# Kernel tuning notes

Hardware: AMD Instinct MI355X
Metric: run time of the kernel (lower is better)

## Reference

```python
import jax, jax.numpy as jnp
import numpy as np

B, S, D, H = 2, 2048, 1024, 16
HD = D // H  # head_dim = 64


def setup_inputs() -> dict:
    key = jax.random.key(0)
    ks = jax.random.split(key, 9)
    scale = 0.02
    x = jax.random.normal(ks[0], (B, S, D), dtype=jnp.float32)
    wq = jax.random.normal(ks[1], (D, D), dtype=jnp.float32) * scale
    bq = jnp.zeros((D,), dtype=jnp.float32)
    wk = jax.random.normal(ks[2], (D, D), dtype=jnp.float32) * scale
    bk = jnp.zeros((D,), dtype=jnp.float32)
    wv = jax.random.normal(ks[3], (D, D), dtype=jnp.float32) * scale
    bv = jnp.zeros((D,), dtype=jnp.float32)
    wo = jax.random.normal(ks[4], (D, D), dtype=jnp.float32) * scale
    bo = jnp.zeros((D,), dtype=jnp.float32)
    # causal mask: 1.0 where key position is in the future of query position
    mask = jnp.triu(jnp.ones((S, S), dtype=jnp.float32), k=1)[None, None]  # [1,1,S,S]
    return {"x": x, "wq": wq, "bq": bq, "wk": wk, "bk": bk,
            "wv": wv, "bv": bv, "wo": wo, "bo": bo, "mask": mask}


def reference(x, wq, bq, wk, bk, wv, bv, wo, bo, mask):
    b, s, d = x.shape
    q = (x @ wq + bq).reshape(b, s, H, HD).transpose(0, 2, 1, 3)  # [b,h,s,hd]
    k = (x @ wk + bk).reshape(b, s, H, HD).transpose(0, 2, 1, 3)
    v = (x @ wv + bv).reshape(b, s, H, HD).transpose(0, 2, 1, 3)
    scores = jnp.einsum('bhqd,bhkd->bhqk', q, k) / jnp.sqrt(jnp.float32(HD))
    scores = scores + mask * (-1e9)
    probs = jax.nn.softmax(scores, axis=-1)
    out = jnp.einsum('bhqk,bhkd->bhqd', probs, v)
    out = out.transpose(0, 2, 1, 3).reshape(b, s, d)
    return out @ wo + bo
```

## Files before the change

### kernel.cpp

```cpp
#include <hip/hip_runtime.h>
#include <hip/hip_bf16.h>
#include <cstdint>

#define DEV static __device__ __forceinline__

typedef unsigned short u16t;
typedef __attribute__((ext_vector_type(4))) float f32x4;
typedef __attribute__((ext_vector_type(4))) unsigned short u16x4;
typedef __attribute__((ext_vector_type(8))) unsigned short u16x8;
typedef __attribute__((ext_vector_type(8))) __bf16 bf16x8;

DEV u16t f2bf(float f) {
  unsigned u = __builtin_bit_cast(unsigned, f);
  u += 0x7fffu + ((u >> 16) & 1u);
  return (u16t)(u >> 16);
}
DEV float bf2f(u16t h) {
  unsigned u = ((unsigned)h) << 16;
  return __builtin_bit_cast(float, u);
}

DEV void gload_lds16(const void* g, void* l) {
  __builtin_amdgcn_global_load_lds(
      (const __attribute__((address_space(1))) void*)g,
      (__attribute__((address_space(3))) void*)l, 16, 0, 0);
}

DEV bf16x8 ldsfrag(const u16t* p) {
  return __builtin_bit_cast(bf16x8, *(const u16x8*)p);
}

__global__ __launch_bounds__(256) void k_convert_x(const float* __restrict__ x,
                                                   u16t* __restrict__ xb) {
  int i = (blockIdx.x * 256 + threadIdx.x) * 4;
  f32x4 v = *(const f32x4*)&x[i];
  u16x4 o;
#pragma unroll
  for (int j = 0; j < 4; ++j) o[j] = f2bf(v[j]);
  *(u16x4*)&xb[i] = o;
}

__global__ __launch_bounds__(256) void k_transw(const float* __restrict__ w0,
                                                const float* __restrict__ w1,
                                                const float* __restrict__ w2,
                                                const float* __restrict__ w3,
                                                u16t* __restrict__ qkvT,
                                                u16t* __restrict__ oT) {
  __shared__ float lds[64][68];
  int z = blockIdx.z;
  const float* W = (z == 0) ? w0 : (z == 1) ? w1 : (z == 2) ? w2 : w3;
  u16t* OUT = (z < 3) ? (qkvT + (size_t)z * 1024 * 1024) : oT;
  int k0 = blockIdx.x * 64, n0 = blockIdx.y * 64;
  int t = threadIdx.x;
  int kl = t >> 4, n4 = (t & 15) << 2;
#pragma unroll
  for (int p = 0; p < 4; ++p) {
    f32x4 v = *(const f32x4*)&W[(size_t)(k0 + kl + p * 16) * 1024 + n0 + n4];
    *(f32x4*)&lds[kl + p * 16][n4] = v;
  }
  __syncthreads();
  int nl = t >> 4, k4 = (t & 15) << 2;
#pragma unroll
  for (int p = 0; p < 4; ++p) {
    int n = nl + p * 16;
    u16x4 o;
#pragma unroll
    for (int i = 0; i < 4; ++i) o[i] = f2bf(lds[k4 + i][n]);
    *(u16x4*)&OUT[(size_t)(n0 + n) * 1024 + k0 + k4] = o;
  }
}

template <bool BF16_OUT>
__global__ __launch_bounds__(256) void k_gemm_bt(const u16t* __restrict__ A,
                                                 const u16t* __restrict__ BT,
                                                 void* __restrict__ Cout,
                                                 const float* __restrict__ b0,
                                                 const float* __restrict__ b1,
                                                 const float* __restrict__ b2,
                                                 int M, int N, int K) {
  __shared__ u16t Al[128 * 64];
  __shared__ u16t Bl[128 * 64];
  const int tid = threadIdx.x;
  const int l = tid & 63;
  const int w = tid >> 6;
  const int m0 = blockIdx.x * 128, n0 = blockIdx.y * 128;
  const int wm = (w >> 1) * 64, wn = (w & 1) * 64;
  const int lm = l & 15, lh = l >> 4;
  f32x4 acc[4][4] = {};

  const int nt = K >> 6;
  for (int t = 0; t < nt; ++t) {
    const int k0 = t << 6;
#pragma unroll
    for (int s = 0; s < 4; ++s) {
      int c = s * 256 + tid;
      int row = c >> 3, slot = c & 7;
      int ks = k0 + (((slot ^ (row & 7)) & 7) << 3);
      gload_lds16(A + (size_t)(m0 + row) * K + ks, &Al[c * 8]);
    }
#pragma unroll
    for (int s = 0; s < 4; ++s) {
      int c = s * 256 + tid;
      int row = c >> 3, slot = c & 7;
      int ks = k0 + (((slot ^ (row & 7)) & 7) << 3);
      gload_lds16(BT + (size_t)(n0 + row) * K + ks, &Bl[c * 8]);
    }
    asm volatile("s_waitcnt vmcnt(0)" ::: "memory");
    __syncthreads();

#pragma unroll
    for (int kk = 0; kk < 2; ++kk) {
      bf16x8 af[4], bfr[4];
#pragma unroll
      for (int i = 0; i < 4; ++i) {
        int ra = wm + i * 16 + lm;
        int sa = (kk * 4 + lh) ^ (ra & 7);
        af[i] = ldsfrag(&Al[ra * 64 + sa * 8]);
        int rb = wn + i * 16 + lm;
        int sb = (kk * 4 + lh) ^ (rb & 7);
        bfr[i] = ldsfrag(&Bl[rb * 64 + sb * 8]);
      }
#pragma unroll
      for (int i = 0; i < 4; ++i)
#pragma unroll
        for (int j = 0; j < 4; ++j)
          acc[i][j] = __builtin_amdgcn_mfma_f32_16x16x32_bf16(af[i], bfr[j],
                                                              acc[i][j], 0, 0, 0);
    }
    __syncthreads();
  }

#pragma unroll
  for (int i = 0; i < 4; ++i) {
    int row = m0 + wm + i * 16 + (lh << 2);
#pragma unroll
    for (int j = 0; j < 4; ++j) {
      int col = n0 + wn + j * 16 + lm;
      const float* bp = (col < 1024) ? b0 : ((col < 2048) ? b1 : b2);
      float bias = bp[col & 1023];
#pragma unroll
      for (int r = 0; r < 4; ++r) {
        float v = acc[i][j][r] + bias;
        if (BF16_OUT)
          ((u16t*)Cout)[(size_t)(row + r) * N + col] = f2bf(v);
        else
          ((float*)Cout)[(size_t)(row + r) * N + col] = v;
      }
    }
  }
}

__global__ __launch_bounds__(256) void k_transv(const u16t* __restrict__ qkv,
                                                u16t* __restrict__ vt) {
  __shared__ u16t lds[64][80];
  int bh = blockIdx.y, b = bh >> 4, h = bh & 15;
  int s0 = blockIdx.x * 64;
  int t = threadIdx.x;
  int sl = t >> 2, d16 = (t & 3) << 4;
  const u16t* src = qkv + (size_t)(b * 2048 + s0 + sl) * 3072 + 2048 + h * 64 + d16;
  *(u16x8*)&lds[sl][d16] = *(const u16x8*)src;
  *(u16x8*)&lds[sl][d16 + 8] = *(const u16x8*)(src + 8);
  __syncthreads();
  int dl = t >> 2, s16 = (t & 3) << 4;
  u16x8 o0, o1;
#pragma unroll
  for (int i = 0; i < 8; ++i) o0[i] = lds[s16 + i][dl];
#pragma unroll
  for (int i = 0; i < 8; ++i) o1[i] = lds[s16 + 8 + i][dl];
  u16t* dst = vt + ((size_t)bh * 64 + dl) * 2048 + s0 + s16;
  *(u16x8*)&dst[0] = o0;
  *(u16x8*)&dst[8] = o1;
}

__global__ __launch_bounds__(256, 4) void k_attn(const u16t* __restrict__ qkv,
                                                 const u16t* __restrict__ vt,
                                                 u16t* __restrict__ outp) {
  __shared__ u16t Kl[2][4096];
  __shared__ u16t Vl[2][4096];
  __shared__ u16t Pl[4][1024];
  const int tid = threadIdx.x, l = tid & 63, w = tid >> 6;
  const int lm = l & 15, lh = l >> 4;
  const int bh = blockIdx.x, b = bh >> 4, h = bh & 15;
  const int y = blockIdx.y;
  const int kg = y >> 3, jj = y & 7;
  const int qt = kg * 8 + ((kg & 1) ? (7 - jj) : jj);
  const int q0 = qt * 64;
  const int nt = qt + 1;

  bf16x8 aq[2];
  const int qrow = q0 + w * 16 + lm;
#pragma unroll
  for (int kk = 0; kk < 2; ++kk) {
    const u16t* src = qkv + (size_t)(b * 2048 + qrow) * 3072 + h * 64 + kk * 32 + lh * 8;
    u16x8 v = *(const u16x8*)src;
    u16x8 o;
#pragma unroll
    for (int e = 0; e < 8; ++e) o[e] = f2bf(bf2f(v[e]) * 0.125f);
    aq[kk] = __builtin_bit_cast(bf16x8, o);
  }

  float mrun = -1e30f;
  float lsum = 0.f;
  f32x4 aco[4] = {};

  const u16t* Kg = qkv + (size_t)b * 2048 * 3072 + 1024 + h * 64;
  const u16t* Vg = vt + (size_t)bh * 64 * 2048;
  u16t* Pw = &Pl[w][0];

  auto stage = [&](int buf, int t) {
#pragma unroll
    for (int s = 0; s < 2; ++s) {
      int c = s * 256 + tid;
      int row = c >> 3, col = ((c & 7) ^ (row & 7)) << 3;
      gload_lds16(Kg + (size_t)(t * 64 + row) * 3072 + col, &Kl[buf][c * 8]);
    }
#pragma unroll
    for (int s = 0; s < 2; ++s) {
      int c = s * 256 + tid;
      int row = c >> 3, col = ((c & 7) ^ (row & 7)) << 3;
      gload_lds16(Vg + (size_t)row * 2048 + t * 64 + col, &Vl[buf][c * 8]);
    }
  };

  stage(0, 0);
  asm volatile("s_waitcnt vmcnt(0)" ::: "memory");
  __syncthreads();

  int buf = 0;
  for (int t = 0; t < nt; ++t) {
    if (t + 1 < nt) stage(buf ^ 1, t + 1);

    f32x4 accs[4] = {};
#pragma unroll
    for (int kk = 0; kk < 2; ++kk) {
      bf16x8 ak[4];
#pragma unroll
      for (int nk = 0; nk < 4; ++nk) {
        int rk = nk * 16 + lm;
        int s16 = (kk * 4 + lh) ^ (rk & 7);
        ak[nk] = ldsfrag(&Kl[buf][rk * 64 + s16 * 8]);
      }
      __builtin_amdgcn_s_setprio(1);
#pragma unroll
      for (int nk = 0; nk < 4; ++nk)
        accs[nk] = __builtin_amdgcn_mfma_f32_16x16x32_bf16(ak[nk], aq[kk],
                                                           accs[nk], 0, 0, 0);
      __builtin_amdgcn_s_setprio(0);
    }

    float vmax = -1e30f;
#pragma unroll
    for (int nk = 0; nk < 4; ++nk)
#pragma unroll
      for (int r = 0; r < 4; ++r) {
        int kvpos = t * 64 + nk * 16 + lh * 4 + r;
        float v = accs[nk][r];
        v = (kvpos > qrow) ? -1e30f : v;
        accs[nk][r] = v;
        vmax = fmaxf(vmax, v);
      }

    if (!__all(vmax <= mrun + 8.f)) {
      float rm = fmaxf(vmax, __shfl_xor(vmax, 16));
      rm = fmaxf(rm, __shfl_xor(rm, 32));
      float mnew = fmaxf(mrun, rm);
      float alpha = __expf(mrun - mnew);
      mrun = mnew;
      lsum *= alpha;
#pragma unroll
      for (int r = 0; r < 4; ++r) {
        float ar = __shfl(alpha, lh * 4 + r);
#pragma unroll
        for (int nd = 0; nd < 4; ++nd) aco[nd][r] *= ar;
      }
    }

#pragma unroll
    for (int nk = 0; nk < 4; ++nk) {
      u16x4 pb;
#pragma unroll
      for (int r = 0; r < 4; ++r) {
        float p = __expf(accs[nk][r] - mrun);
        lsum += p;
        pb[r] = f2bf(p);
      }
      int s16 = (nk * 2 + (lh >> 1)) ^ (lm & 7);
      *(u16x4*)&Pw[lm * 64 + s16 * 8 + (lh & 1) * 4] = pb;
    }

#pragma unroll
    for (int kk = 0; kk < 2; ++kk) {
      int s16p = (kk * 4 + lh) ^ (lm & 7);
      bf16x8 ap = ldsfrag(&Pw[lm * 64 + s16p * 8]);
      __builtin_amdgcn_s_setprio(1);
#pragma unroll
      for (int nd = 0; nd < 4; ++nd) {
        int rv = nd * 16 + lm;
        int s16v = (kk * 4 + lh) ^ (rv & 7);
        bf16x8 bv = ldsfrag(&Vl[buf][rv * 64 + s16v * 8]);
        aco[nd] = __builtin_amdgcn_mfma_f32_16x16x32_bf16(ap, bv, aco[nd], 0, 0, 0);
      }
      __builtin_amdgcn_s_setprio(0);
    }

    asm volatile("s_waitcnt vmcnt(0)" ::: "memory");
    __syncthreads();
    buf ^= 1;
  }

  lsum += __shfl_xor(lsum, 16);
  lsum += __shfl_xor(lsum, 32);
  float inv = 1.0f / lsum;
#pragma unroll
  for (int r = 0; r < 4; ++r) {
    float ir = __shfl(inv, lh * 4 + r);
    int row = q0 + w * 16 + lh * 4 + r;
#pragma unroll
    for (int nd = 0; nd < 4; ++nd) {
      int col = h * 64 + nd * 16 + lm;
      outp[(size_t)(b * 2048 + row) * 1024 + col] = f2bf(aco[nd][r] * ir);
    }
  }
}

extern "C" void kernel_launch(void* const* d_in, const int* in_sizes, int n_in,
                              void* d_out, int out_size, void* d_ws, size_t ws_size,
                              hipStream_t stream) {
  const float* x = (const float*)d_in[0];
  const float* wq = (const float*)d_in[1];
  const float* bq = (const float*)d_in[2];
  const float* wk = (const float*)d_in[3];
  const float* bk = (const float*)d_in[4];
  const float* wv = (const float*)d_in[5];
  const float* bv = (const float*)d_in[6];
  const float* wo = (const float*)d_in[7];
  const float* bo = (const float*)d_in[8];

  char* ws = (char*)d_ws;
  u16t* xb = (u16t*)ws;
  u16t* wqkvT = (u16t*)(ws + (8u << 20));
  u16t* woT = (u16t*)(ws + (14u << 20));
  u16t* qkv = (u16t*)(ws + (16u << 20));
  u16t* vt = (u16t*)(ws + (40u << 20));
  u16t* attn_out = xb;

  k_convert_x<<<4096, 256, 0, stream>>>(x, xb);
  k_transw<<<dim3(16, 16, 4), 256, 0, stream>>>(wq, wk, wv, wo, wqkvT, woT);
  k_gemm_bt<true><<<dim3(32, 24), 256, 0, stream>>>(xb, wqkvT, qkv, bq, bk, bv,
                                                    4096, 3072, 1024);
  k_transv<<<dim3(32, 32), 256, 0, stream>>>(qkv, vt);
  k_attn<<<dim3(32, 32), 256, 0, stream>>>(qkv, vt, attn_out);
  k_gemm_bt<false><<<dim3(32, 8), 256, 0, stream>>>(attn_out, woT, d_out, bo, bo,
                                                    bo, 4096, 1024, 1024);
}
```

Before: 130.1 us.

## Fuse V transpose into QKV GEMM epilogue and restructure attention blocks

The QKV GEMM epilogue now writes the V columns straight into the transposed [b,h,d,s] layout, which removes the separate transpose kernel and its extra pass over memory. The attention kernel drops to 128 threads, and each wave now handles 32 query rows with two MFMA streams that share every K/V fragment load. Each block processes a pair of causal query tiles (jp and 31-jp) to balance work, and the causal mask is applied only on the diagonal tile. P is packed with v_cvt_pk_bf16_f32. In exchange there are fewer blocks and more registers per wave, and the V epilogue stores are strided 8-byte writes.

```diff
diff --git a/kernel.cpp b/kernel.cpp
--- a/kernel.cpp
+++ b/kernel.cpp
@@ -70,13 +70,14 @@
   }
 }
 
-template <bool BF16_OUT>
+template <bool BF16_OUT, bool VSPLIT>
 __global__ __launch_bounds__(256) void k_gemm_bt(const u16t* __restrict__ A,
                                                  const u16t* __restrict__ BT,
                                                  void* __restrict__ Cout,
                                                  const float* __restrict__ b0,
                                                  const float* __restrict__ b1,
                                                  const float* __restrict__ b2,
+                                                 u16t* __restrict__ vt,
                                                  int M, int N, int K) {
   __shared__ u16t Al[128 * 64];
   __shared__ u16t Bl[128 * 64];
@@ -130,195 +131,231 @@
     __syncthreads();
   }
 
-#pragma unroll
-  for (int i = 0; i < 4; ++i) {
-    int row = m0 + wm + i * 16 + (lh << 2);
+  if (!VSPLIT || (n0 + wn) < 2048) {
+#pragma unroll
+    for (int i = 0; i < 4; ++i) {
+      int row = m0 + wm + i * 16 + (lh << 2);
+#pragma unroll
+      for (int j = 0; j < 4; ++j) {
+        int col = n0 + wn + j * 16 + lm;
+        const float* bp = (col < 1024) ? b0 : ((col < 2048) ? b1 : b2);
+        float bias = bp[col & 1023];
+#pragma unroll
+        for (int r = 0; r < 4; ++r) {
+          float v = acc[i][j][r] + bias;
+          if (BF16_OUT)
+            ((u16t*)Cout)[(size_t)(row + r) * N + col] = f2bf(v);
+          else
+            ((float*)Cout)[(size_t)(row + r) * N + col] = v;
+        }
+      }
+    }
+  } else {
+#pragma unroll
+    for (int i = 0; i < 4; ++i) {
+      int row = m0 + wm + i * 16 + (lh << 2);
+      int bidx = row >> 11, s0 = row & 2047;
 #pragma unroll
     for (int j = 0; j < 4; ++j) {
-      int col = n0 + wn + j * 16 + lm;
-      const float* bp = (col < 1024) ? b0 : ((col < 2048) ? b1 : b2);
-      float bias = bp[col & 1023];
-#pragma unroll
-      for (int r = 0; r < 4; ++r) {
-        float v = acc[i][j][r] + bias;
-        if (BF16_OUT)
-          ((u16t*)Cout)[(size_t)(row + r) * N + col] = f2bf(v);
-        else
-          ((float*)Cout)[(size_t)(row + r) * N + col] = v;
-      }
-    }
-  }
-}
-
-__global__ __launch_bounds__(256) void k_transv(const u16t* __restrict__ qkv,
-                                                u16t* __restrict__ vt) {
-  __shared__ u16t lds[64][80];
-  int bh = blockIdx.y, b = bh >> 4, h = bh & 15;
-  int s0 = blockIdx.x * 64;
-  int t = threadIdx.x;
-  int sl = t >> 2, d16 = (t & 3) << 4;
-  const u16t* src = qkv + (size_t)(b * 2048 + s0 + sl) * 3072 + 2048 + h * 64 + d16;
-  *(u16x8*)&lds[sl][d16] = *(const u16x8*)src;
-  *(u16x8*)&lds[sl][d16 + 8] = *(const u16x8*)(src + 8);
-  __syncthreads();
-  int dl = t >> 2, s16 = (t & 3) << 4;
-  u16x8 o0, o1;
-#pragma unroll
-  for (int i = 0; i < 8; ++i) o0[i] = lds[s16 + i][dl];
-#pragma unroll
-  for (int i = 0; i < 8; ++i) o1[i] = lds[s16 + 8 + i][dl];
-  u16t* dst = vt + ((size_t)bh * 64 + dl) * 2048 + s0 + s16;
-  *(u16x8*)&dst[0] = o0;
-  *(u16x8*)&dst[8] = o1;
-}
-
-__global__ __launch_bounds__(256, 4) void k_attn(const u16t* __restrict__ qkv,
-                                                 const u16t* __restrict__ vt,
-                                                 u16t* __restrict__ outp) {
+        int col = n0 + wn + j * 16 + lm;
+        int d = col - 2048;
+        int hh = d >> 6, dd = d & 63;
+        float bias = b2[d];
+        u16x4 o;
+#pragma unroll
+        for (int r = 0; r < 4; ++r) o[r] = f2bf(acc[i][j][r] + bias);
+        *(u16x4*)&vt[((size_t)((bidx * 16 + hh) * 64 + dd)) * 2048 + s0] = o;
+      }
+    }
+  }
+}
+
+__global__ __launch_bounds__(128) void k_attn(const u16t* __restrict__ qkv,
+                                              const u16t* __restrict__ vt,
+                                              u16t* __restrict__ outp) {
   __shared__ u16t Kl[2][4096];
   __shared__ u16t Vl[2][4096];
-  __shared__ u16t Pl[4][1024];
+  __shared__ u16t Pl[2][2][1024];
   const int tid = threadIdx.x, l = tid & 63, w = tid >> 6;
   const int lm = l & 15, lh = l >> 4;
   const int bh = blockIdx.x, b = bh >> 4, h = bh & 15;
-  const int y = blockIdx.y;
-  const int kg = y >> 3, jj = y & 7;
-  const int qt = kg * 8 + ((kg & 1) ? (7 - jj) : jj);
-  const int q0 = qt * 64;
-  const int nt = qt + 1;
-
-  bf16x8 aq[2];
-  const int qrow = q0 + w * 16 + lm;
-#pragma unroll
-  for (int kk = 0; kk < 2; ++kk) {
-    const u16t* src = qkv + (size_t)(b * 2048 + qrow) * 3072 + h * 64 + kk * 32 + lh * 8;
-    u16x8 v = *(const u16x8*)src;
-    u16x8 o;
-#pragma unroll
-    for (int e = 0; e < 8; ++e) o[e] = f2bf(bf2f(v[e]) * 0.125f);
-    aq[kk] = __builtin_bit_cast(bf16x8, o);
-  }
-
-  float mrun = -1e30f;
-  float lsum = 0.f;
-  f32x4 aco[4] = {};
+  const int jp = blockIdx.y;
 
   const u16t* Kg = qkv + (size_t)b * 2048 * 3072 + 1024 + h * 64;
   const u16t* Vg = vt + (size_t)bh * 64 * 2048;
-  u16t* Pw = &Pl[w][0];
-
-  auto stage = [&](int buf, int t) {
-#pragma unroll
-    for (int s = 0; s < 2; ++s) {
-      int c = s * 256 + tid;
-      int row = c >> 3, col = ((c & 7) ^ (row & 7)) << 3;
-      gload_lds16(Kg + (size_t)(t * 64 + row) * 3072 + col, &Kl[buf][c * 8]);
-    }
-#pragma unroll
-    for (int s = 0; s < 2; ++s) {
-      int c = s * 256 + tid;
-      int row = c >> 3, col = ((c & 7) ^ (row & 7)) << 3;
-      gload_lds16(Vg + (size_t)row * 2048 + t * 64 + col, &Vl[buf][c * 8]);
+
+  auto stage = [&](int bb, int t) {
+#pragma unroll
+    for (int s = 0; s < 4; ++s) {
+      int c = s * 128 + tid;
+      int row = c >> 3, slot = c & 7;
+      int col = ((slot ^ (row & 7)) & 7) << 3;
+      gload_lds16(Kg + (size_t)(t * 64 + row) * 3072 + col, &Kl[bb][c * 8]);
+    }
+#pragma unroll
+    for (int s = 0; s < 4; ++s) {
+      int c = s * 128 + tid;
+      int row = c >> 3, slot = c & 7;
+      int col = ((slot ^ (row & 7)) & 7) << 3;
+      gload_lds16(Vg + (size_t)row * 2048 + t * 64 + col, &Vl[bb][c * 8]);
     }
   };
 
-  stage(0, 0);
-  asm volatile("s_waitcnt vmcnt(0)" ::: "memory");
-  __syncthreads();
-
-  int buf = 0;
-  for (int t = 0; t < nt; ++t) {
-    if (t + 1 < nt) stage(buf ^ 1, t + 1);
-
-    f32x4 accs[4] = {};
-#pragma unroll
-    for (int kk = 0; kk < 2; ++kk) {
-      bf16x8 ak[4];
-#pragma unroll
-      for (int nk = 0; nk < 4; ++nk) {
-        int rk = nk * 16 + lm;
-        int s16 = (kk * 4 + lh) ^ (rk & 7);
-        ak[nk] = ldsfrag(&Kl[buf][rk * 64 + s16 * 8]);
-      }
-      __builtin_amdgcn_s_setprio(1);
-#pragma unroll
-      for (int nk = 0; nk < 4; ++nk)
-        accs[nk] = __builtin_amdgcn_mfma_f32_16x16x32_bf16(ak[nk], aq[kk],
-                                                           accs[nk], 0, 0, 0);
-      __builtin_amdgcn_s_setprio(0);
-    }
-
-    float vmax = -1e30f;
-#pragma unroll
-    for (int nk = 0; nk < 4; ++nk)
-#pragma unroll
-      for (int r = 0; r < 4; ++r) {
-        int kvpos = t * 64 + nk * 16 + lh * 4 + r;
-        float v = accs[nk][r];
-        v = (kvpos > qrow) ? -1e30f : v;
-        accs[nk][r] = v;
-        vmax = fmaxf(vmax, v);
-      }
-
-    if (!__all(vmax <= mrun + 8.f)) {
-      float rm = fmaxf(vmax, __shfl_xor(vmax, 16));
-      rm = fmaxf(rm, __shfl_xor(rm, 32));
-      float mnew = fmaxf(mrun, rm);
-      float alpha = __expf(mrun - mnew);
-      mrun = mnew;
-      lsum *= alpha;
-#pragma unroll
-      for (int r = 0; r < 4; ++r) {
-        float ar = __shfl(alpha, lh * 4 + r);
-#pragma unroll
-        for (int nd = 0; nd < 4; ++nd) aco[nd][r] *= ar;
-      }
-    }
-
-#pragma unroll
-    for (int nk = 0; nk < 4; ++nk) {
-      u16x4 pb;
-#pragma unroll
-      for (int r = 0; r < 4; ++r) {
-        float p = __expf(accs[nk][r] - mrun);
-        lsum += p;
-        pb[r] = f2bf(p);
-      }
-      int s16 = (nk * 2 + (lh >> 1)) ^ (lm & 7);
-      *(u16x4*)&Pw[lm * 64 + s16 * 8 + (lh & 1) * 4] = pb;
-    }
-
-#pragma unroll
-    for (int kk = 0; kk < 2; ++kk) {
-      int s16p = (kk * 4 + lh) ^ (lm & 7);
-      bf16x8 ap = ldsfrag(&Pw[lm * 64 + s16p * 8]);
-      __builtin_amdgcn_s_setprio(1);
-#pragma unroll
-      for (int nd = 0; nd < 4; ++nd) {
-        int rv = nd * 16 + lm;
-        int s16v = (kk * 4 + lh) ^ (rv & 7);
-        bf16x8 bv = ldsfrag(&Vl[buf][rv * 64 + s16v * 8]);
-        aco[nd] = __builtin_amdgcn_mfma_f32_16x16x32_bf16(ap, bv, aco[nd], 0, 0, 0);
-      }
-      __builtin_amdgcn_s_setprio(0);
-    }
-
+  for (int half = 0; half < 2; ++half) {
+    const int qt = half ? (31 - jp) : jp;
+    const int q0 = qt * 64;
+    const int nt = qt + 1;
+    const int qbase = q0 + w * 32;
+
+    bf16x8 aq[2][2];
+#pragma unroll
+    for (int qm = 0; qm < 2; ++qm)
+#pragma unroll
+      for (int kk = 0; kk < 2; ++kk) {
+        const u16t* src = qkv + (size_t)(b * 2048 + qbase + qm * 16 + lm) * 3072 +
+                          h * 64 + kk * 32 + lh * 8;
+        u16x8 v = *(const u16x8*)src;
+        u16x8 o;
+#pragma unroll
+        for (int e = 0; e < 8; ++e) o[e] = f2bf(bf2f(v[e]) * 0.125f);
+        aq[qm][kk] = __builtin_bit_cast(bf16x8, o);
+      }
+
+    float mrun[2] = {-1e30f, -1e30f};
+    float lsum[2] = {0.f, 0.f};
+    f32x4 aco[2][4] = {};
+    const int qr0 = qbase + lm, qr1 = qbase + 16 + lm;
+
+    stage(0, 0);
     asm volatile("s_waitcnt vmcnt(0)" ::: "memory");
     __syncthreads();
-    buf ^= 1;
-  }
-
-  lsum += __shfl_xor(lsum, 16);
-  lsum += __shfl_xor(lsum, 32);
-  float inv = 1.0f / lsum;
-#pragma unroll
-  for (int r = 0; r < 4; ++r) {
-    float ir = __shfl(inv, lh * 4 + r);
-    int row = q0 + w * 16 + lh * 4 + r;
-#pragma unroll
-    for (int nd = 0; nd < 4; ++nd) {
-      int col = h * 64 + nd * 16 + lm;
-      outp[(size_t)(b * 2048 + row) * 1024 + col] = f2bf(aco[nd][r] * ir);
+
+    int buf = 0;
+    for (int t = 0; t < nt; ++t) {
+      if (t + 1 < nt) stage(buf ^ 1, t + 1);
+
+      f32x4 accs[2][4] = {};
+#pragma unroll
+      for (int kk = 0; kk < 2; ++kk) {
+        bf16x8 ak[4];
+#pragma unroll
+        for (int nk = 0; nk < 4; ++nk) {
+          int rk = nk * 16 + lm;
+          int s16 = (kk * 4 + lh) ^ (rk & 7);
+          ak[nk] = ldsfrag(&Kl[buf][rk * 64 + s16 * 8]);
+        }
+        __builtin_amdgcn_s_setprio(1);
+#pragma unroll
+        for (int nk = 0; nk < 4; ++nk) {
+          accs[0][nk] = __builtin_amdgcn_mfma_f32_16x16x32_bf16(ak[nk], aq[0][kk],
+                                                                accs[0][nk], 0, 0, 0);
+          accs[1][nk] = __builtin_amdgcn_mfma_f32_16x16x32_bf16(ak[nk], aq[1][kk],
+                                                                accs[1][nk], 0, 0, 0);
+        }
+        __builtin_amdgcn_s_setprio(0);
+      }
+
+      float vmax[2] = {-1e30f, -1e30f};
+      if (t == nt - 1) {
+#pragma unroll
+        for (int nk = 0; nk < 4; ++nk)
+#pragma unroll
+          for (int r = 0; r < 4; ++r) {
+            int kvpos = t * 64 + nk * 16 + lh * 4 + r;
+            float v0 = accs[0][nk][r];
+            v0 = (kvpos > qr0) ? -1e30f : v0;
+            accs[0][nk][r] = v0;
+            vmax[0] = fmaxf(vmax[0], v0);
+            float v1 = accs[1][nk][r];
+            v1 = (kvpos > qr1) ? -1e30f : v1;
+            accs[1][nk][r] = v1;
+            vmax[1] = fmaxf(vmax[1], v1);
+          }
+      } else {
+#pragma unroll
+        for (int nk = 0; nk < 4; ++nk)
+#pragma unroll
+          for (int r = 0; r < 4; ++r) {
+            vmax[0] = fmaxf(vmax[0], accs[0][nk][r]);
+            vmax[1] = fmaxf(vmax[1], accs[1][nk][r]);
+          }
+      }
+
+      if (!__all((vmax[0] <= mrun[0] + 8.f) & (vmax[1] <= mrun[1] + 8.f))) {
+#pragma unroll
+        for (int qm = 0; qm < 2; ++qm) {
+          float rm = fmaxf(vmax[qm], __shfl_xor(vmax[qm], 16));
+          rm = fmaxf(rm, __shfl_xor(rm, 32));
+          float mnew = fmaxf(mrun[qm], rm);
+          float alpha = __expf(mrun[qm] - mnew);
+          mrun[qm] = mnew;
+          lsum[qm] *= alpha;
+#pragma unroll
+          for (int r = 0; r < 4; ++r) {
+            float ar = __shfl(alpha, lh * 4 + r);
+#pragma unroll
+            for (int nd = 0; nd < 4; ++nd) aco[qm][nd][r] *= ar;
+          }
+        }
+      }
+
+#pragma unroll
+      for (int qm = 0; qm < 2; ++qm) {
+        u16t* Pw = &Pl[w][qm][0];
+#pragma unroll
+        for (int nk = 0; nk < 4; ++nk) {
+          float p0 = __expf(accs[qm][nk][0] - mrun[qm]);
+          float p1 = __expf(accs[qm][nk][1] - mrun[qm]);
+          float p2 = __expf(accs[qm][nk][2] - mrun[qm]);
+          float p3 = __expf(accs[qm][nk][3] - mrun[qm]);
+          lsum[qm] += (p0 + p1) + (p2 + p3);
+          unsigned wlo, whi;
+          asm("v_cvt_pk_bf16_f32 %0, %1, %2" : "=v"(wlo) : "v"(p0), "v"(p1));
+          asm("v_cvt_pk_bf16_f32 %0, %1, %2" : "=v"(whi) : "v"(p2), "v"(p3));
+          int off = lm * 64 + ((((2 * nk + (lh >> 1)) ^ (lm & 7)) & 7) << 3) +
+                    ((lh & 1) << 2);
+          *(uint2*)&Pw[off] = make_uint2(wlo, whi);
+        }
+      }
+
+#pragma unroll
+      for (int kk = 0; kk < 2; ++kk) {
+        int sp = (kk * 4 + lh) ^ (lm & 7);
+        bf16x8 ap0 = ldsfrag(&Pl[w][0][lm * 64 + sp * 8]);
+        bf16x8 ap1 = ldsfrag(&Pl[w][1][lm * 64 + sp * 8]);
+        __builtin_amdgcn_s_setprio(1);
+#pragma unroll
+        for (int nd = 0; nd < 4; ++nd) {
+          int rv = nd * 16 + lm;
+          int sv = (kk * 4 + lh) ^ (rv & 7);
+          bf16x8 bv = ldsfrag(&Vl[buf][rv * 64 + sv * 8]);
+          aco[0][nd] = __builtin_amdgcn_mfma_f32_16x16x32_bf16(ap0, bv, aco[0][nd], 0, 0, 0);
+          aco[1][nd] = __builtin_amdgcn_mfma_f32_16x16x32_bf16(ap1, bv, aco[1][nd], 0, 0, 0);
+        }
+        __builtin_amdgcn_s_setprio(0);
+      }
+
+      asm volatile("s_waitcnt vmcnt(0)" ::: "memory");
+      __syncthreads();
+      buf ^= 1;
+    }
+
+#pragma unroll
+    for (int qm = 0; qm < 2; ++qm) {
+      float ls = lsum[qm];
+      ls += __shfl_xor(ls, 16);
+      ls += __shfl_xor(ls, 32);
+      float inv = 1.0f / ls;
+#pragma unroll
+      for (int r = 0; r < 4; ++r) {
+        float ir = __shfl(inv, lh * 4 + r);
+        int row = q0 + w * 32 + qm * 16 + lh * 4 + r;
+#pragma unroll
+        for (int nd = 0; nd < 4; ++nd) {
+          int col = h * 64 + nd * 16 + lm;
+          outp[(size_t)(b * 2048 + row) * 1024 + col] = f2bf(aco[qm][nd][r] * ir);
+        }
+      }
     }
   }
 }
@@ -346,10 +383,9 @@
 
   k_convert_x<<<4096, 256, 0, stream>>>(x, xb);
   k_transw<<<dim3(16, 16, 4), 256, 0, stream>>>(wq, wk, wv, wo, wqkvT, woT);
-  k_gemm_bt<true><<<dim3(32, 24), 256, 0, stream>>>(xb, wqkvT, qkv, bq, bk, bv,
-                                                    4096, 3072, 1024);
-  k_transv<<<dim3(32, 32), 256, 0, stream>>>(qkv, vt);
-  k_attn<<<dim3(32, 32), 256, 0, stream>>>(qkv, vt, attn_out);
-  k_gemm_bt<false><<<dim3(32, 8), 256, 0, stream>>>(attn_out, woT, d_out, bo, bo,
-                                                    bo, 4096, 1024, 1024);
-}
+  k_gemm_bt<true, true><<<dim3(32, 24), 256, 0, stream>>>(xb, wqkvT, qkv, bq, bk,
+                                                          bv, vt, 4096, 3072, 1024);
+  k_attn<<<dim3(32, 16), 128, 0, stream>>>(qkv, vt, attn_out);
+  k_gemm_bt<false, false><<<dim3(32, 8), 256, 0, stream>>>(
+      attn_out, woT, d_out, bo, bo, bo, nullptr, 4096, 1024, 1024);
+}
```

New measurement: 140.7 us. 8.1% more time.
